# Optimization experiments

Hardware: AMD Instinct MI355X
Metric: run time of the kernel (lower is better)

The kernel has to match this reference:

```python
import jax, jax.numpy as jnp
import numpy as np

EMBED_DIM = 1024
NUM_HEADS = 16
HEAD_DIM = EMBED_DIM // NUM_HEADS
B, N = 4, 2048


def setup_inputs() -> dict:
    key = jax.random.key(0)
    k = jax.random.split(key, 5)
    scale = 1.0 / np.sqrt(EMBED_DIM)
    return {
        "x": jax.random.normal(k[0], (B, N, EMBED_DIM), dtype=jnp.float32),
        # torch nn.Linear convention: y = x @ W.T + b, W shape [out, in]
        "qkv_w": jax.random.uniform(k[1], (3 * EMBED_DIM, EMBED_DIM), jnp.float32, -scale, scale),
        "qkv_b": jax.random.uniform(k[2], (3 * EMBED_DIM,), jnp.float32, -scale, scale),
        "out_w": jax.random.uniform(k[3], (EMBED_DIM, EMBED_DIM), jnp.float32, -scale, scale),
        "out_b": jax.random.uniform(k[4], (EMBED_DIM,), jnp.float32, -scale, scale),
    }


def reference(x, qkv_w, qkv_b, out_w, out_b):
    b, n, e = x.shape
    qkv = x @ qkv_w.T + qkv_b                      # [B,N,3E]
    qkv = qkv.reshape(b, n, 3, NUM_HEADS, HEAD_DIM)
    qkv = jnp.transpose(qkv, (2, 0, 3, 1, 4))      # [3,B,H,N,D]
    q, k, v = qkv[0], qkv[1], qkv[2]
    scores = jnp.einsum("bhqd,bhkd->bhqk", q, k) / np.sqrt(HEAD_DIM)
    weights = jax.nn.softmax(scores, axis=-1)
    attn = jnp.einsum("bhqk,bhkd->bhqd", weights, v)  # [B,H,N,D]
    attn = jnp.transpose(attn, (0, 2, 1, 3)).reshape(b, n, e)
    return attn @ out_w.T + out_b
```

## Files before the change

kernel.cpp:

```cpp
#include <hip/hip_runtime.h>
#include <hip/hip_bf16.h>

#define EMBED 1024
#define NHEADS 16
#define HDIM 64
#define BATCH 4
#define SEQ 2048
#define MROWS (BATCH*SEQ)
#define QKVN (3*EMBED)
#define KDIM 1024

typedef __bf16 bf16;
typedef __bf16 bf16x4 __attribute__((ext_vector_type(4)));
typedef __bf16 bf16x8 __attribute__((ext_vector_type(8)));
typedef float f32x4 __attribute__((ext_vector_type(4)));
typedef float f32x16 __attribute__((ext_vector_type(16)));

#define QSCALE 0.18033688011112042f

__global__ void cvt_bf16(const float* __restrict__ src, bf16* __restrict__ dst, int n4) {
    int i = blockIdx.x * blockDim.x + threadIdx.x;
    if (i < n4) {
        float4 f = ((const float4*)src)[i];
        bf16x4 o;
        o[0] = (bf16)f.x; o[1] = (bf16)f.y; o[2] = (bf16)f.z; o[3] = (bf16)f.w;
        *((bf16x4*)dst + i) = o;
    }
}

template<int MODE>
__launch_bounds__(256)
__global__ void gemm_bt(const bf16* __restrict__ A, const bf16* __restrict__ B,
                        const float* __restrict__ bias,
                        float* __restrict__ outF,
                        bf16* __restrict__ Qb, bf16* __restrict__ Kb, bf16* __restrict__ Vt)
{
    __shared__ bf16 Alds[128][32];
    __shared__ bf16 Blds[128][32];
    const int tid = threadIdx.x;
    const int l = tid & 63, w = tid >> 6;
    const int wr = w >> 1, wc = w & 1;
    const int tM = blockIdx.y * 128, tN = blockIdx.x * 128;

    f32x4 acc[4][4] = {};
    const bf16* Abase = A + (size_t)tM * KDIM;
    const bf16* Bbase = B + (size_t)tN * KDIM;

    for (int k0 = 0; k0 < KDIM; k0 += 32) {
        #pragma unroll
        for (int t = 0; t < 2; ++t) {
            int idx = t * 256 + tid;
            int row = idx >> 2;
            int kc = (idx & 3) * 8;
            __builtin_amdgcn_global_load_lds(
                (const __attribute__((address_space(1))) void*)(Abase + (size_t)row * KDIM + k0 + kc),
                (__attribute__((address_space(3))) void*)((char*)&Alds[0][0] + idx * 16),
                16, 0, 0);
            __builtin_amdgcn_global_load_lds(
                (const __attribute__((address_space(1))) void*)(Bbase + (size_t)row * KDIM + k0 + kc),
                (__attribute__((address_space(3))) void*)((char*)&Blds[0][0] + idx * 16),
                16, 0, 0);
        }
        __syncthreads();
        bf16x8 a[4], b[4];
        #pragma unroll
        for (int i = 0; i < 4; ++i)
            a[i] = *(const bf16x8*)&Alds[wr * 64 + i * 16 + (l & 15)][(l >> 4) * 8];
        #pragma unroll
        for (int j = 0; j < 4; ++j)
            b[j] = *(const bf16x8*)&Blds[wc * 64 + j * 16 + (l & 15)][(l >> 4) * 8];
        #pragma unroll
        for (int i = 0; i < 4; ++i)
            #pragma unroll
            for (int j = 0; j < 4; ++j)
                acc[i][j] = __builtin_amdgcn_mfma_f32_16x16x32_bf16(a[i], b[j], acc[i][j], 0, 0, 0);
        __syncthreads();
    }

    #pragma unroll
    for (int i = 0; i < 4; ++i) {
        #pragma unroll
        for (int j = 0; j < 4; ++j) {
            int n = tN + wc * 64 + j * 16 + (l & 15);
            float bv = bias[n];
            #pragma unroll
            for (int r = 0; r < 4; ++r) {
                int m = tM + wr * 64 + i * 16 + (l >> 4) * 4 + r;
                float v = acc[i][j][r] + bv;
                if (MODE == 1) {
                    outF[(size_t)m * EMBED + n] = v;
                } else {
                    int which = n >> 10, nn = n & 1023;
                    int hd = nn >> 6, d = nn & 63;
                    int bidx = m >> 11, ns = m & 2047;
                    int bh = bidx * NHEADS + hd;
                    int t32 = ns >> 5;
                    if (which == 2) {
                        int rem16 = ns & 15;
                        int c = (ns >> 4) & 1;
                        int fj = (rem16 & 3) | ((rem16 & 8) >> 1);
                        int fhi = (rem16 >> 2) & 1;
                        int dblk = d >> 5;
                        int lane = (d & 31) | (fhi << 5);
                        size_t idx = ((((size_t)bh * 64 + t32) * 2 + dblk) * 2 + c) * 512 + lane * 8 + fj;
                        Vt[idx] = (bf16)v;
                    } else {
                        int kk = d >> 4, fhi = (d >> 3) & 1, fj = d & 7;
                        int lane = (ns & 31) | (fhi << 5);
                        size_t idx = (((size_t)bh * 64 + t32) * 4 + kk) * 512 + lane * 8 + fj;
                        if (which == 0) Qb[idx] = (bf16)(v * QSCALE);
                        else            Kb[idx] = (bf16)v;
                    }
                }
            }
        }
    }
}

__launch_bounds__(256)
__global__ void attn_kernel(const bf16* __restrict__ Qb, const bf16* __restrict__ Kb,
                            const bf16* __restrict__ Vt, bf16* __restrict__ AO)
{
    const int tid = threadIdx.x, l = tid & 63, w = tid >> 6;
    const int lo5 = l & 31, hi = l >> 5;
    int bid = blockIdx.x;
    int swz = (bid & 7) * 128 + (bid >> 3);
    const int bh = swz >> 4;
    const int qt = swz & 15;

    const bf16* QFh = Qb + (size_t)bh * (64 * 2048);
    const bf16* KFh = Kb + (size_t)bh * (64 * 2048);
    const bf16* VFh = Vt + (size_t)bh * (64 * 2048);

    const int qtile = qt * 4 + w;
    const bf16* qbase = QFh + (size_t)qtile * 2048 + (size_t)l * 8;
    bf16x8 qf[4];
    #pragma unroll
    for (int kk = 0; kk < 4; ++kk)
        qf[kk] = *(const bf16x8*)(qbase + kk * 512);

    f32x16 O0 = {}, O1 = {};
    f32x16 psum = {};

    bf16x8 kA0, kA1, kA2, kA3, kB0, kB1, kB2, kB3;
    {
        const bf16* kb0 = KFh + (size_t)l * 8;
        kA0 = *(const bf16x8*)(kb0);
        kA1 = *(const bf16x8*)(kb0 + 512);
        kA2 = *(const bf16x8*)(kb0 + 1024);
        kA3 = *(const bf16x8*)(kb0 + 1536);
    }

#define ATTN_BODY(KV, KC0, KC1, KC2, KC3, KN0, KN1, KN2, KN3)                           \
    {                                                                                    \
        const int kv0 = (KV);                                                            \
                   \
        const bf16* vbase = VFh + (size_t)(kv0 >> 5) * 2048 + (size_t)l * 8;             \
        bf16x8 vf00 = *(const bf16x8*)(vbase);                                           \
        bf16x8 vf01 = *(const bf16x8*)(vbase + 512);                                     \
        bf16x8 vf10 = *(const bf16x8*)(vbase + 1024);                                    \
        bf16x8 vf11 = *(const bf16x8*)(vbase + 1536);                                    \
                 \
        int kn = kv0 + 32; kn = (kn < SEQ) ? kn : 0;                                     \
        const bf16* knb = KFh + (size_t)(kn >> 5) * 2048 + (size_t)l * 8;                \
        KN0 = *(const bf16x8*)(knb);                                                     \
        KN1 = *(const bf16x8*)(knb + 512);                                               \
        KN2 = *(const bf16x8*)(knb + 1024);                                              \
        KN3 = *(const bf16x8*)(knb + 1536);                                              \
                                  \
        f32x16 S = {};                                                                   \
        __builtin_amdgcn_s_setprio(1);                                                   \
        S = __builtin_amdgcn_mfma_f32_32x32x16_bf16(KC0, qf[0], S, 0, 0, 0);             \
        S = __builtin_amdgcn_mfma_f32_32x32x16_bf16(KC1, qf[1], S, 0, 0, 0);             \
        S = __builtin_amdgcn_mfma_f32_32x32x16_bf16(KC2, qf[2], S, 0, 0, 0);             \
        S = __builtin_amdgcn_mfma_f32_32x32x16_bf16(KC3, qf[3], S, 0, 0, 0);             \
        __builtin_amdgcn_s_setprio(0);                                                   \
                                     \
        f32x16 P;                                                                        \
        _Pragma("unroll")                                                                \
        for (int r = 0; r < 16; ++r)                                                     \
            P[r] = __builtin_amdgcn_exp2f(S[r]);                                         \
        psum += P;                                                                       \
        bf16x8 pa0, pa1;                                                                 \
        _Pragma("unroll")                                                                \
        for (int r = 0; r < 8; ++r) { pa0[r] = (bf16)P[r]; pa1[r] = (bf16)P[r + 8]; }    \
        __builtin_amdgcn_s_setprio(1);                                                   \
        O0 = __builtin_amdgcn_mfma_f32_32x32x16_bf16(vf00, pa0, O0, 0, 0, 0);            \
        O0 = __builtin_amdgcn_mfma_f32_32x32x16_bf16(vf01, pa1, O0, 0, 0, 0);            \
        O1 = __builtin_amdgcn_mfma_f32_32x32x16_bf16(vf10, pa0, O1, 0, 0, 0);            \
        O1 = __builtin_amdgcn_mfma_f32_32x32x16_bf16(vf11, pa1, O1, 0, 0, 0);            \
        __builtin_amdgcn_s_setprio(0);                                                   \
    }

    for (int kv = 0; kv < SEQ; kv += 64) {
        ATTN_BODY(kv,      kA0, kA1, kA2, kA3, kB0, kB1, kB2, kB3)
        ATTN_BODY(kv + 32, kB0, kB1, kB2, kB3, kA0, kA1, kA2, kA3)
    }
#undef ATTN_BODY

    float s0 = (psum[0] + psum[1]) + (psum[2] + psum[3]);
    float s1 = (psum[4] + psum[5]) + (psum[6] + psum[7]);
    float s2 = (psum[8] + psum[9]) + (psum[10] + psum[11]);
    float s3 = (psum[12] + psum[13]) + (psum[14] + psum[15]);
    float tot = (s0 + s1) + (s2 + s3);
    tot += __shfl_xor(tot, 32);
    float linv = 1.0f / tot;

    const int b = bh >> 4, hd = bh & 15;
    const int q0 = qt * 128 + w * 32;
    bf16* outp = &AO[(size_t)(b * SEQ + q0 + lo5) * EMBED + hd * HDIM];
    #pragma unroll
    for (int g = 0; g < 4; ++g) {
        bf16x4 o0, o1;
        #pragma unroll
        for (int r4 = 0; r4 < 4; ++r4) {
            o0[r4] = (bf16)(O0[g * 4 + r4] * linv);
            o1[r4] = (bf16)(O1[g * 4 + r4] * linv);
        }
        *(bf16x4*)&outp[g * 8 + hi * 4] = o0;
        *(bf16x4*)&outp[32 + g * 8 + hi * 4] = o1;
    }
}

extern "C" void kernel_launch(void* const* d_in, const int* in_sizes, int n_in,
                              void* d_out, int out_size, void* d_ws, size_t ws_size,
                              hipStream_t stream) {
    const float* x     = (const float*)d_in[0];
    const float* qkv_w = (const float*)d_in[1];
    const float* qkv_b = (const float*)d_in[2];
    const float* out_w = (const float*)d_in[3];
    const float* out_b = (const float*)d_in[4];
    float* out = (float*)d_out;

    char* ws = (char*)d_ws;
    bf16* xb  = (bf16*)(ws);
    bf16* qwb = (bf16*)(ws + 16777216);
    bf16* owb = (bf16*)(ws + 23068672);
    bf16* Qb  = (bf16*)(ws + 25165824);
    bf16* Kb  = (bf16*)(ws + 41943040);
    bf16* Vt  = (bf16*)(ws + 58720256);
    bf16* AO  = (bf16*)(ws + 75497472);

    cvt_bf16<<<(MROWS * EMBED / 4 + 255) / 256, 256, 0, stream>>>(x, xb, MROWS * EMBED / 4);
    cvt_bf16<<<(QKVN * KDIM / 4 + 255) / 256, 256, 0, stream>>>(qkv_w, qwb, QKVN * KDIM / 4);
    cvt_bf16<<<(EMBED * KDIM / 4 + 255) / 256, 256, 0, stream>>>(out_w, owb, EMBED * KDIM / 4);

    gemm_bt<0><<<dim3(QKVN / 128, MROWS / 128), 256, 0, stream>>>(
        xb, qwb, qkv_b, nullptr, Qb, Kb, Vt);

    attn_kernel<<<BATCH * NHEADS * (SEQ / 128), 256, 0, stream>>>(Qb, Kb, Vt, AO);

    gemm_bt<1><<<dim3(EMBED / 128, MROWS / 128), 256, 0, stream>>>(
        AO, owb, out_b, out, nullptr, nullptr, nullptr);
}
```

Measured before the change: 206.5 us.

## Software-pipeline QK^T one tile ahead in attention and fuse conversion kernels

```diff
diff --git a/kernel.cpp b/kernel.cpp
--- a/kernel.cpp
+++ b/kernel.cpp
@@ -18,14 +18,22 @@
 
 #define QSCALE 0.18033688011112042f
 
-__global__ void cvt_bf16(const float* __restrict__ src, bf16* __restrict__ dst, int n4) {
+#define NX (MROWS*EMBED/4)
+#define NQ (QKVN*KDIM/4)
+#define NO (EMBED*KDIM/4)
+__global__ void cvt_all(const float* __restrict__ x, const float* __restrict__ qw,
+                        const float* __restrict__ ow,
+                        bf16* __restrict__ xb, bf16* __restrict__ qwb, bf16* __restrict__ owb) {
     int i = blockIdx.x * blockDim.x + threadIdx.x;
-    if (i < n4) {
-        float4 f = ((const float4*)src)[i];
-        bf16x4 o;
-        o[0] = (bf16)f.x; o[1] = (bf16)f.y; o[2] = (bf16)f.z; o[3] = (bf16)f.w;
-        *((bf16x4*)dst + i) = o;
-    }
+    const float* src; bf16* dst; int j;
+    if (i < NX)            { src = x;  dst = xb;  j = i; }
+    else if (i < NX + NQ)  { src = qw; dst = qwb; j = i - NX; }
+    else if (i < NX+NQ+NO) { src = ow; dst = owb; j = i - NX - NQ; }
+    else return;
+    float4 f = ((const float4*)src)[j];
+    bf16x4 o;
+    o[0] = (bf16)f.x; o[1] = (bf16)f.y; o[2] = (bf16)f.z; o[3] = (bf16)f.w;
+    *((bf16x4*)dst + j) = o;
 }
 
 template<int MODE>
@@ -117,6 +125,12 @@
     }
 }
 
+static __device__ __forceinline__ unsigned cvt_pk(float lo, float hi) {
+    unsigned r;
+    asm("v_cvt_pk_bf16_f32 %0, %1, %2" : "=v"(r) : "v"(lo), "v"(hi));
+    return r;
+}
+
 __launch_bounds__(256)
 __global__ void attn_kernel(const bf16* __restrict__ Qb, const bf16* __restrict__ Kb,
                             const bf16* __restrict__ Vt, bf16* __restrict__ AO)
@@ -129,8 +143,8 @@
     const int qt = swz & 15;
 
     const bf16* QFh = Qb + (size_t)bh * (64 * 2048);
-    const bf16* KFh = Kb + (size_t)bh * (64 * 2048);
-    const bf16* VFh = Vt + (size_t)bh * (64 * 2048);
+    const bf16* Kit = Kb + (size_t)bh * (64 * 2048) + (size_t)l * 8;
+    const bf16* Vit = Vt + (size_t)bh * (64 * 2048) + (size_t)l * 8;
 
     const int qtile = qt * 4 + w;
     const bf16* qbase = QFh + (size_t)qtile * 2048 + (size_t)l * 8;
@@ -140,71 +154,77 @@
         qf[kk] = *(const bf16x8*)(qbase + kk * 512);
 
     f32x16 O0 = {}, O1 = {};
-    f32x16 psum = {};
-
-    bf16x8 kA0, kA1, kA2, kA3, kB0, kB1, kB2, kB3;
-    {
-        const bf16* kb0 = KFh + (size_t)l * 8;
-        kA0 = *(const bf16x8*)(kb0);
-        kA1 = *(const bf16x8*)(kb0 + 512);
-        kA2 = *(const bf16x8*)(kb0 + 1024);
-        kA3 = *(const bf16x8*)(kb0 + 1536);
-    }
-
-#define ATTN_BODY(KV, KC0, KC1, KC2, KC3, KN0, KN1, KN2, KN3)                           \
+    float lsum = 0.f;
+
+    bf16x8 kK0, kK1, kK2, kK3;
+    kK0 = *(const bf16x8*)(Kit);
+    kK1 = *(const bf16x8*)(Kit + 512);
+    kK2 = *(const bf16x8*)(Kit + 1024);
+    kK3 = *(const bf16x8*)(Kit + 1536);
+    f32x16 SA, SB;
+    #pragma unroll
+    for (int r = 0; r < 16; ++r) SA[r] = 0.f;
+    SA = __builtin_amdgcn_mfma_f32_32x32x16_bf16(kK0, qf[0], SA, 0, 0, 0);
+    SA = __builtin_amdgcn_mfma_f32_32x32x16_bf16(kK1, qf[1], SA, 0, 0, 0);
+    SA = __builtin_amdgcn_mfma_f32_32x32x16_bf16(kK2, qf[2], SA, 0, 0, 0);
+    SA = __builtin_amdgcn_mfma_f32_32x32x16_bf16(kK3, qf[3], SA, 0, 0, 0);
+    kK0 = *(const bf16x8*)(Kit + 2048);
+    kK1 = *(const bf16x8*)(Kit + 2048 + 512);
+    kK2 = *(const bf16x8*)(Kit + 2048 + 1024);
+    kK3 = *(const bf16x8*)(Kit + 2048 + 1536);
+
+#define ATTN_BODY(T, SCUR, SNXT)                                                        \
     {                                                                                    \
-        const int kv0 = (KV);                                                            \
-                   \
-        const bf16* vbase = VFh + (size_t)(kv0 >> 5) * 2048 + (size_t)l * 8;             \
-        bf16x8 vf00 = *(const bf16x8*)(vbase);                                           \
-        bf16x8 vf01 = *(const bf16x8*)(vbase + 512);                                     \
-        bf16x8 vf10 = *(const bf16x8*)(vbase + 1024);                                    \
-        bf16x8 vf11 = *(const bf16x8*)(vbase + 1536);                                    \
-                 \
-        int kn = kv0 + 32; kn = (kn < SEQ) ? kn : 0;                                     \
-        const bf16* knb = KFh + (size_t)(kn >> 5) * 2048 + (size_t)l * 8;                \
-        KN0 = *(const bf16x8*)(knb);                                                     \
-        KN1 = *(const bf16x8*)(knb + 512);                                               \
-        KN2 = *(const bf16x8*)(knb + 1024);                                              \
-        KN3 = *(const bf16x8*)(knb + 1536);                                              \
-                                  \
-        f32x16 S = {};                                                                   \
+        const int t = (T);                                                               \
+        const bf16* vb = Vit + (size_t)t * 2048;                                         \
+        bf16x8 vf00 = *(const bf16x8*)(vb);                                              \
+        bf16x8 vf01 = *(const bf16x8*)(vb + 512);                                        \
+        bf16x8 vf10 = *(const bf16x8*)(vb + 1024);                                       \
+        bf16x8 vf11 = *(const bf16x8*)(vb + 1536);                                       \
         __builtin_amdgcn_s_setprio(1);                                                   \
-        S = __builtin_amdgcn_mfma_f32_32x32x16_bf16(KC0, qf[0], S, 0, 0, 0);             \
-        S = __builtin_amdgcn_mfma_f32_32x32x16_bf16(KC1, qf[1], S, 0, 0, 0);             \
-        S = __builtin_amdgcn_mfma_f32_32x32x16_bf16(KC2, qf[2], S, 0, 0, 0);             \
-        S = __builtin_amdgcn_mfma_f32_32x32x16_bf16(KC3, qf[3], S, 0, 0, 0);             \
+        _Pragma("unroll")                                                                \
+        for (int r = 0; r < 16; ++r) SNXT[r] = 0.f;                                      \
+        SNXT = __builtin_amdgcn_mfma_f32_32x32x16_bf16(kK0, qf[0], SNXT, 0, 0, 0);       \
+        SNXT = __builtin_amdgcn_mfma_f32_32x32x16_bf16(kK1, qf[1], SNXT, 0, 0, 0);       \
+        SNXT = __builtin_amdgcn_mfma_f32_32x32x16_bf16(kK2, qf[2], SNXT, 0, 0, 0);       \
+        SNXT = __builtin_amdgcn_mfma_f32_32x32x16_bf16(kK3, qf[3], SNXT, 0, 0, 0);       \
         __builtin_amdgcn_s_setprio(0);                                                   \
-                                     \
-        f32x16 P;                                                                        \
+        int tp = t + 2; tp = (tp < 64) ? tp : 0;                                         \
+        const bf16* kb = Kit + (size_t)tp * 2048;                                        \
+        kK0 = *(const bf16x8*)(kb);                                                      \
+        kK1 = *(const bf16x8*)(kb + 512);                                                \
+        kK2 = *(const bf16x8*)(kb + 1024);                                               \
+        kK3 = *(const bf16x8*)(kb + 1536);                                               \
+        float p[16];                                                                     \
         _Pragma("unroll")                                                                \
         for (int r = 0; r < 16; ++r)                                                     \
-            P[r] = __builtin_amdgcn_exp2f(S[r]);                                         \
-        psum += P;                                                                       \
-        bf16x8 pa0, pa1;                                                                 \
-        _Pragma("unroll")                                                                \
-        for (int r = 0; r < 8; ++r) { pa0[r] = (bf16)P[r]; pa1[r] = (bf16)P[r + 8]; }    \
+            p[r] = __builtin_amdgcn_exp2f(SCUR[r]);                                      \
+        float s0 = (p[0] + p[1]) + (p[2] + p[3]);                                        \
+        float s1 = (p[4] + p[5]) + (p[6] + p[7]);                                        \
+        float s2 = (p[8] + p[9]) + (p[10] + p[11]);                                      \
+        float s3 = (p[12] + p[13]) + (p[14] + p[15]);                                    \
+        lsum += (s0 + s1) + (s2 + s3);                                                   \
+        union { unsigned u[4]; bf16x8 v; } pk0, pk1;                                     \
+        pk0.u[0] = cvt_pk(p[0], p[1]);   pk0.u[1] = cvt_pk(p[2], p[3]);                  \
+        pk0.u[2] = cvt_pk(p[4], p[5]);   pk0.u[3] = cvt_pk(p[6], p[7]);                  \
+        pk1.u[0] = cvt_pk(p[8], p[9]);   pk1.u[1] = cvt_pk(p[10], p[11]);                \
+        pk1.u[2] = cvt_pk(p[12], p[13]); pk1.u[3] = cvt_pk(p[14], p[15]);                \
         __builtin_amdgcn_s_setprio(1);                                                   \
-        O0 = __builtin_amdgcn_mfma_f32_32x32x16_bf16(vf00, pa0, O0, 0, 0, 0);            \
-        O0 = __builtin_amdgcn_mfma_f32_32x32x16_bf16(vf01, pa1, O0, 0, 0, 0);            \
-        O1 = __builtin_amdgcn_mfma_f32_32x32x16_bf16(vf10, pa0, O1, 0, 0, 0);            \
-        O1 = __builtin_amdgcn_mfma_f32_32x32x16_bf16(vf11, pa1, O1, 0, 0, 0);            \
+        O0 = __builtin_amdgcn_mfma_f32_32x32x16_bf16(vf00, pk0.v, O0, 0, 0, 0);          \
+        O0 = __builtin_amdgcn_mfma_f32_32x32x16_bf16(vf01, pk1.v, O0, 0, 0, 0);          \
+        O1 = __builtin_amdgcn_mfma_f32_32x32x16_bf16(vf10, pk0.v, O1, 0, 0, 0);          \
+        O1 = __builtin_amdgcn_mfma_f32_32x32x16_bf16(vf11, pk1.v, O1, 0, 0, 0);          \
         __builtin_amdgcn_s_setprio(0);                                                   \
     }
 
-    for (int kv = 0; kv < SEQ; kv += 64) {
-        ATTN_BODY(kv,      kA0, kA1, kA2, kA3, kB0, kB1, kB2, kB3)
-        ATTN_BODY(kv + 32, kB0, kB1, kB2, kB3, kA0, kA1, kA2, kA3)
+    for (int t2 = 0; t2 < 64; t2 += 2) {
+        ATTN_BODY(t2,     SA, SB)
+        ATTN_BODY(t2 + 1, SB, SA)
     }
 #undef ATTN_BODY
 
-    float s0 = (psum[0] + psum[1]) + (psum[2] + psum[3]);
-    float s1 = (psum[4] + psum[5]) + (psum[6] + psum[7]);
-    float s2 = (psum[8] + psum[9]) + (psum[10] + psum[11]);
-    float s3 = (psum[12] + psum[13]) + (psum[14] + psum[15]);
-    float tot = (s0 + s1) + (s2 + s3);
-    tot += __shfl_xor(tot, 32);
-    float linv = 1.0f / tot;
+    lsum += __shfl_xor(lsum, 32);
+    float linv = 1.0f / lsum;
 
     const int b = bh >> 4, hd = bh & 15;
     const int q0 = qt * 128 + w * 32;
@@ -241,9 +261,7 @@
     bf16* Vt  = (bf16*)(ws + 58720256);
     bf16* AO  = (bf16*)(ws + 75497472);
 
-    cvt_bf16<<<(MROWS * EMBED / 4 + 255) / 256, 256, 0, stream>>>(x, xb, MROWS * EMBED / 4);
-    cvt_bf16<<<(QKVN * KDIM / 4 + 255) / 256, 256, 0, stream>>>(qkv_w, qwb, QKVN * KDIM / 4);
-    cvt_bf16<<<(EMBED * KDIM / 4 + 255) / 256, 256, 0, stream>>>(out_w, owb, EMBED * KDIM / 4);
+    cvt_all<<<(NX + NQ + NO + 255) / 256, 256, 0, stream>>>(x, qkv_w, out_w, xb, qwb, owb);
 
     gemm_bt<0><<<dim3(QKVN / 128, MROWS / 128), 256, 0, stream>>>(
         xb, qwb, qkv_b, nullptr, Qb, Kb, Vt);
```

New measurement: 201.7 us. 1.02x faster.
